# Optimization experiments

Hardware: AMD Instinct MI355X
Metric: run time of the kernel (lower is better)

Reference implementation:

```python
import jax, jax.numpy as jnp
import numpy as np


def setup_inputs() -> dict:
    key = jax.random.key(0)
    ks = jax.random.split(key, 5)
    B, O4, K = 8, 1024, 4096  # batch, output_number//4, 8*8*256//4
    N = 4 * K  # input feature dim = 16384
    # Glorot-uniform-ish scale for (O4*4, N) effective fan
    scale = jnp.sqrt(2.0 / (N + 4 * O4)).astype(jnp.float32)
    x = jax.random.normal(ks[0], (B, N), dtype=jnp.float32)
    w1 = jax.random.normal(ks[1], (B, O4, K), dtype=jnp.float32) * scale
    w2 = jax.random.normal(ks[2], (B, O4, K), dtype=jnp.float32) * scale
    w3 = jax.random.normal(ks[3], (B, O4, K), dtype=jnp.float32) * scale
    w4 = jax.random.normal(ks[4], (B, O4, K), dtype=jnp.float32) * scale
    return {"x": x, "w1": w1, "w2": w2, "w3": w3, "w4": w4}


def reference(x, w1, w2, w3, w4):
    # first_row: (B, O4, N) with N = 4*K
    first_row = jnp.concatenate([w1, w2, w3, w4], axis=-1)
    N = x.shape[-1]
    shift = N // 4
    # Original: W = concat([roll(first_row, i*shift, axis=-1) for i in range(4)], axis=1)
    #           out = squeeze(W @ x[..., None])  -> (B, 4*O4)
    # Equivalent without materializing W: roll(W, s) @ x == W @ roll(x, -s)
    outs = [
        jnp.einsum('bon,bn->bo', first_row, jnp.roll(x, -i * shift, axis=-1))
        for i in range(4)
    ]
    return jnp.concatenate(outs, axis=-1)  # (B, 4*O4)
```

## Files before the change

### kernel.cpp

```cpp
#include <hip/hip_runtime.h>


#define B_DIM 8
#define O4_DIM 1024
#define K_DIM 4096
#define N_DIM 16384
#define TILE_O 4

typedef float floatx4 __attribute__((ext_vector_type(4)));

__global__ __launch_bounds__(256) void eq_dense_kernel(
    const float* __restrict__ x,
    const float* __restrict__ w1,
    const float* __restrict__ w2,
    const float* __restrict__ w3,
    const float* __restrict__ w4,
    float* __restrict__ out)
{
    const int b    = blockIdx.y;
    const int o0   = blockIdx.x * TILE_O;
    const int tid  = threadIdx.x;
    const int j    = tid >> 6;
    const int lane = tid & 63;

    __shared__ floatx4 xs[N_DIM / 4];
    __shared__ float red[4][TILE_O][4];

    {
        const floatx4* xg = reinterpret_cast<const floatx4*>(x + (size_t)b * N_DIM);
#pragma unroll
        for (int r = 0; r < 16; ++r)
            xs[r * 256 + tid] = xg[r * 256 + tid];
    }
    __syncthreads();

    const float* wsel = (j == 0) ? w1 : (j == 1) ? w2 : (j == 2) ? w3 : w4;
    const floatx4* wbase = reinterpret_cast<const floatx4*>(
        wsel + ((size_t)b * O4_DIM + o0) * K_DIM);

    float acc[TILE_O][4];
#pragma unroll
    for (int o = 0; o < TILE_O; ++o)
#pragma unroll
        for (int m = 0; m < 4; ++m)
            acc[o][m] = 0.0f;

#pragma unroll 4
    for (int it = 0; it < 16; ++it) {
        const int idx = it * 64 + lane;
        floatx4 wv[TILE_O];
#pragma unroll
        for (int o = 0; o < TILE_O; ++o)
            wv[o] = wbase[o * 1024 + idx];
        floatx4 xv[4];
#pragma unroll
        for (int m = 0; m < 4; ++m)
            xv[m] = xs[m * 1024 + idx];
#pragma unroll
        for (int o = 0; o < TILE_O; ++o)
#pragma unroll
            for (int m = 0; m < 4; ++m) {
                acc[o][m] += wv[o].x * xv[m].x;
                acc[o][m] += wv[o].y * xv[m].y;
                acc[o][m] += wv[o].z * xv[m].z;
                acc[o][m] += wv[o].w * xv[m].w;
            }
    }

#pragma unroll
    for (int o = 0; o < TILE_O; ++o)
#pragma unroll
        for (int m = 0; m < 4; ++m) {
            float v = acc[o][m];
            v += __shfl_xor(v, 32, 64);
            v += __shfl_xor(v, 16, 64);
            v += __shfl_xor(v, 8, 64);
            v += __shfl_xor(v, 4, 64);
            v += __shfl_xor(v, 2, 64);
            v += __shfl_xor(v, 1, 64);
            acc[o][m] = v;
        }

    __syncthreads();
    if (lane == 0) {
#pragma unroll
        for (int o = 0; o < TILE_O; ++o)
#pragma unroll
            for (int m = 0; m < 4; ++m)
                red[j][o][m] = acc[o][m];
    }
    __syncthreads();

    if (tid < TILE_O * 4) {
        const int o = tid & (TILE_O - 1);
        const int i = tid >> 2;
        float v = 0.0f;
#pragma unroll
        for (int jj = 0; jj < 4; ++jj)
            v += red[jj][o][(i + jj) & 3];
        out[(size_t)b * (4 * O4_DIM) + (size_t)i * O4_DIM + (o0 + o)] = v;
    }
}

extern "C" void kernel_launch(void* const* d_in, const int* in_sizes, int n_in,
                              void* d_out, int out_size, void* d_ws, size_t ws_size,
                              hipStream_t stream) {
    const float* x  = (const float*)d_in[0];
    const float* w1 = (const float*)d_in[1];
    const float* w2 = (const float*)d_in[2];
    const float* w3 = (const float*)d_in[3];
    const float* w4 = (const float*)d_in[4];
    float* out = (float*)d_out;

    dim3 grid(O4_DIM / TILE_O, B_DIM);
    dim3 block(256);
    eq_dense_kernel<<<grid, block, 0, stream>>>(x, w1, w2, w3, w4, out);
}
```

Before: 94.05 us.

## Split the K reduction into slices with atomic accumulation and a smaller x tile

Launches a 3D grid that splits the K dimension into four slices. Each block stages only its slice of x in shared memory (16KB instead of 64KB) and adds its partial results into the zero-initialised output with atomicAdd. The aim is higher occupancy and less redundant x staging per block, so the bandwidth-bound weight stream keeps more loads in flight. The cost is an extra memset launch, atomic traffic, and a non-deterministic floating-point summation order.

Measured after the change: 101.8 us. +8.2%, slower.

```diff
diff --git a/kernel.cpp b/kernel.cpp
--- a/kernel.cpp
+++ b/kernel.cpp
@@ -6,10 +6,12 @@
 #define K_DIM 4096
 #define N_DIM 16384
 #define TILE_O 4
+#define SLICES 4
+#define SLICE_F4 256
 
 typedef float floatx4 __attribute__((ext_vector_type(4)));
 
-__global__ __launch_bounds__(256) void eq_dense_kernel(
+__global__ __launch_bounds__(256) void eq_dense_slice_kernel(
     const float* __restrict__ x,
     const float* __restrict__ w1,
     const float* __restrict__ w2,
@@ -17,26 +19,28 @@
     const float* __restrict__ w4,
     float* __restrict__ out)
 {
-    const int b    = blockIdx.y;
-    const int o0   = blockIdx.x * TILE_O;
+    const int ot   = blockIdx.x;
+    const int s    = blockIdx.y;
+    const int b    = blockIdx.z;
+    const int o0   = ot * TILE_O;
     const int tid  = threadIdx.x;
     const int j    = tid >> 6;
     const int lane = tid & 63;
 
-    __shared__ floatx4 xs[N_DIM / 4];
+    __shared__ floatx4 xs[4 * SLICE_F4];
     __shared__ float red[4][TILE_O][4];
 
     {
         const floatx4* xg = reinterpret_cast<const floatx4*>(x + (size_t)b * N_DIM);
 #pragma unroll
-        for (int r = 0; r < 16; ++r)
-            xs[r * 256 + tid] = xg[r * 256 + tid];
+        for (int m = 0; m < 4; ++m)
+            xs[m * SLICE_F4 + tid] = xg[m * 1024 + s * SLICE_F4 + tid];
     }
     __syncthreads();
 
     const float* wsel = (j == 0) ? w1 : (j == 1) ? w2 : (j == 2) ? w3 : w4;
     const floatx4* wbase = reinterpret_cast<const floatx4*>(
-        wsel + ((size_t)b * O4_DIM + o0) * K_DIM);
+        wsel + ((size_t)b * O4_DIM + o0) * K_DIM) + s * SLICE_F4;
 
     float acc[TILE_O][4];
 #pragma unroll
@@ -45,8 +49,8 @@
         for (int m = 0; m < 4; ++m)
             acc[o][m] = 0.0f;
 
-#pragma unroll 4
-    for (int it = 0; it < 16; ++it) {
+#pragma unroll
+    for (int it = 0; it < 4; ++it) {
         const int idx = it * 64 + lane;
         floatx4 wv[TILE_O];
 #pragma unroll
@@ -55,7 +59,7 @@
         floatx4 xv[4];
 #pragma unroll
         for (int m = 0; m < 4; ++m)
-            xv[m] = xs[m * 1024 + idx];
+            xv[m] = xs[m * SLICE_F4 + idx];
 #pragma unroll
         for (int o = 0; o < TILE_O; ++o)
 #pragma unroll
@@ -81,7 +85,6 @@
             acc[o][m] = v;
         }
 
-    __syncthreads();
     if (lane == 0) {
 #pragma unroll
         for (int o = 0; o < TILE_O; ++o)
@@ -91,14 +94,14 @@
     }
     __syncthreads();
 
-    if (tid < TILE_O * 4) {
-        const int o = tid & (TILE_O - 1);
+    if (tid < 16) {
+        const int o = tid & 3;
         const int i = tid >> 2;
         float v = 0.0f;
 #pragma unroll
         for (int jj = 0; jj < 4; ++jj)
             v += red[jj][o][(i + jj) & 3];
-        out[(size_t)b * (4 * O4_DIM) + (size_t)i * O4_DIM + (o0 + o)] = v;
+        atomicAdd(&out[(size_t)b * (4 * O4_DIM) + (size_t)i * O4_DIM + (o0 + o)], v);
     }
 }
 
@@ -112,7 +115,9 @@
     const float* w4 = (const float*)d_in[4];
     float* out = (float*)d_out;
 
-    dim3 grid(O4_DIM / TILE_O, B_DIM);
+    hipMemsetAsync(out, 0, (size_t)out_size * sizeof(float), stream);
+
+    dim3 grid(O4_DIM / TILE_O, SLICES, B_DIM);
     dim3 block(256);
-    eq_dense_kernel<<<grid, block, 0, stream>>>(x, w1, w2, w3, w4, out);
+    eq_dense_slice_kernel<<<grid, block, 0, stream>>>(x, w1, w2, w3, w4, out);
 }
```
